# Kernel optimization log

Hardware: AMD Instinct MI355X
Metric: run time of the kernel (lower is better)

Reference implementation:

```python
import jax, jax.numpy as jnp
import numpy as np

N = 50000
E = 800000
H, C = 8, 16          # heads, per-head channels (H*C = 128)
G = 64                # number of graphs
EPS = 1e-5


def setup_inputs() -> dict:
    key = jax.random.key(0)
    ks = jax.random.split(key, 8)
    x = jax.random.normal(ks[0], (N, 128), dtype=jnp.float32)
    edge_index = jax.random.randint(ks[1], (2, E), 0, N, dtype=jnp.int64)
    batch = jnp.sort(jax.random.randint(ks[2], (N,), 0, G, dtype=jnp.int64))
    W = jax.random.normal(ks[3], (3, 128, 128), dtype=jnp.float32) * 0.08
    att_src = jax.random.normal(ks[4], (3, H, C), dtype=jnp.float32) * 0.1
    att_dst = jax.random.normal(ks[5], (3, H, C), dtype=jnp.float32) * 0.1
    bias = jnp.zeros((3, 128), dtype=jnp.float32)
    gamma = jnp.ones((3, 128), dtype=jnp.float32)
    beta = jnp.zeros((3, 128), dtype=jnp.float32)
    ro_w = jax.random.normal(ks[6], (128, 2), dtype=jnp.float32) * 0.08
    ro_b = jnp.zeros((2,), dtype=jnp.float32)
    return {"x": x, "edge_index": edge_index, "batch": batch, "W": W,
            "att_src": att_src, "att_dst": att_dst, "bias": bias,
            "gamma": gamma, "beta": beta, "ro_w": ro_w, "ro_b": ro_b}


def _gat_block(prev, h, src, dst, W, a_s, a_d, b, g, be):
    # GATConv (concat=True, add_self_loops already applied to src/dst)
    xp = (h @ W).reshape(N, H, C)                       # [N,H,C]
    al_s = jnp.sum(xp * a_s, axis=-1)                   # [N,H]
    al_d = jnp.sum(xp * a_d, axis=-1)                   # [N,H]
    logits = jax.nn.leaky_relu(al_s[src] + al_d[dst], negative_slope=0.2)  # [Et,H]
    m = jax.ops.segment_max(logits, dst, num_segments=N)        # softmax over dst groups
    ex = jnp.exp(logits - m[dst])
    denom = jax.ops.segment_sum(ex, dst, num_segments=N)
    alpha = ex / denom[dst]                              # [Et,H]
    msg = xp[src] * alpha[:, :, None]                    # [Et,H,C]
    agg = jax.ops.segment_sum(msg, dst, num_segments=N).reshape(N, H * C) + b
    y = prev + agg
    # BatchNorm1d (training mode: batch stats, biased variance)
    mu = y.mean(axis=0)
    var = y.var(axis=0)
    yn = (y - mu) / jnp.sqrt(var + EPS) * g + be
    return jax.nn.elu(yn)


def reference(x, edge_index, batch, W, att_src, att_dst, bias, gamma, beta, ro_w, ro_b):
    loops = jnp.arange(N, dtype=edge_index.dtype)
    src = jnp.concatenate([edge_index[0], loops])        # PyG add_self_loops=True
    dst = jnp.concatenate([edge_index[1], loops])
    h = x
    prev = jnp.zeros((N, 128), dtype=x.dtype)
    for i in range(3):
        out = _gat_block(prev, h, src, dst, W[i], att_src[i], att_dst[i],
                         bias[i], gamma[i], beta[i])
        prev = h[:, :128]
        h = out
    # global mean pool over graphs
    sums = jax.ops.segment_sum(h, batch, num_segments=G)
    cnt = jax.ops.segment_sum(jnp.ones((N,), dtype=h.dtype), batch, num_segments=G)
    pooled = sums / jnp.maximum(cnt, 1.0)[:, None]
    return pooled @ ro_w + ro_b
```

## Files before the change

kernel.cpp:

```cpp
#include <hip/hip_runtime.h>
#include <hip/hip_bf16.h>
#include <math.h>

#define NN 50000
#define EE 800000
#define MM (EE + NN)
#define GG 64
#define SWG 512
#define NSB ((NN + 255) / 256)
#define PSP 16

__device__ __forceinline__ int geti(const void* p, long idx, int is64) {
    return is64 ? (int)((const long long*)p)[idx] : ((const int*)p)[idx];
}

__device__ __forceinline__ float bf2f(unsigned short u) {
    return __uint_as_float(((unsigned)u) << 16);
}

__device__ __forceinline__ float eluf(float z) {
    return z > 0.f ? z : expm1f(z);
}


__global__ void k_zero(int* p, int n, const int* __restrict__ ei, int* __restrict__ flag) {
    int i = blockIdx.x * blockDim.x + threadIdx.x;
    if (i < n) p[i] = 0;
    if (blockIdx.x == 0 && threadIdx.x == 0 && ei != nullptr) {
        int ok = 1;
        for (int k = 0; k < 128; ++k) {
            int lo = ei[2 * k], hi = ei[2 * k + 1];
            if (hi != 0 || (unsigned)lo >= (unsigned)NN) { ok = 0; break; }
        }
        flag[0] = ok;
    }
}

__global__ void k_count(const void* __restrict__ ei, const int* __restrict__ flag,
                        int* __restrict__ counts) {
    int e = blockIdx.x * blockDim.x + threadIdx.x;
    if (e >= MM) return;
    int is64 = flag[0];
    int d = (e < EE) ? geti(ei, (long)EE + e, is64) : (e - EE);
    if ((unsigned)d < (unsigned)NN) atomicAdd(&counts[d], 1);
}

__global__ __launch_bounds__(256) void k_scan1(const int* __restrict__ counts,
                                               int* __restrict__ rowptr,
                                               int* __restrict__ bsum) {
    __shared__ int buf[256];
    int b = blockIdx.x, tid = threadIdx.x;
    int i = b * 256 + tid;
    int v = (i < NN) ? counts[i] : 0;
    buf[tid] = v;
    __syncthreads();
    for (int off = 1; off < 256; off <<= 1) {
        int t = (tid >= off) ? buf[tid - off] : 0;
        __syncthreads();
        buf[tid] += t;
        __syncthreads();
    }
    if (i < NN) rowptr[i + 1] = buf[tid];
    if (tid == 255) bsum[b] = buf[255];
}

__global__ __launch_bounds__(256) void k_scan2(int* __restrict__ bsum) {
    __shared__ int buf[256];
    int tid = threadIdx.x;
    int v = (tid < NSB) ? bsum[tid] : 0;
    buf[tid] = v;
    __syncthreads();
    for (int off = 1; off < 256; off <<= 1) {
        int t = (tid >= off) ? buf[tid - off] : 0;
        __syncthreads();
        buf[tid] += t;
        __syncthreads();
    }
    if (tid < NSB) bsum[tid] = (tid == 0) ? 0 : buf[tid - 1];
}

__global__ __launch_bounds__(256) void k_scan3(int* __restrict__ rowptr,
                                               const int* __restrict__ bsum) {
    int b = blockIdx.x, tid = threadIdx.x;
    int i = b * 256 + tid;
    if (i < NN) rowptr[i + 1] += bsum[b];
    if (b == 0 && tid == 0) rowptr[0] = 0;
}

__global__ void k_fill(const void* __restrict__ ei, const int* __restrict__ flag,
                       const int* __restrict__ rowptr,
                       int* __restrict__ fill, int* __restrict__ colv) {
    int e = blockIdx.x * blockDim.x + threadIdx.x;
    if (e >= MM) return;
    int is64 = flag[0];
    int s, d;
    if (e < EE) { s = geti(ei, e, is64); d = geti(ei, (long)EE + e, is64); }
    else { s = d = e - EE; }
    if ((unsigned)d >= (unsigned)NN || (unsigned)s >= (unsigned)NN) return;
    int pos = rowptr[d] + atomicAdd(&fill[d], 1);
    if ((unsigned)pos < (unsigned)MM) colv[pos] = s;
}


__global__ __launch_bounds__(256) void k_gemm_att(
    const float* __restrict__ hsrc, const float* __restrict__ Ysrc,
    const float* __restrict__ st, const float* __restrict__ W,
    const float* __restrict__ attS, const float* __restrict__ attD,
    unsigned short* __restrict__ xpb, float* __restrict__ als,
    float* __restrict__ ald, int n)
{
    __shared__ float Wt[32][8][12];
    __shared__ float Ht[128][34];
    int tid = threadIdx.x;
    int hh = tid & 7;
    int r0 = tid >> 3;
    int rbase = (blockIdx.x >> 1) * 128;
    int cbase = (blockIdx.x & 1) * 64;
    bool useY = (Ysrc != nullptr);

    float acc[4][8];
#pragma unroll
    for (int a = 0; a < 4; ++a)
#pragma unroll
        for (int b = 0; b < 8; ++b) acc[a][b] = 0.f;

    for (int k0 = 0; k0 < 128; k0 += 32) {
#pragma unroll
        for (int jj = 0; jj < 2; ++jj) {
            int idx = tid * 2 + jj;
            int kk = idx >> 4;
            int cpos = (idx & 15) * 4;
            int h2 = cpos >> 3, t = cpos & 7;
            *(float4*)&Wt[kk][h2][t] =
                *(const float4*)&W[(k0 + kk) * 128 + cbase + h2 * 8 + t];
        }
#pragma unroll
        for (int j = 0; j < 4; ++j) {
            int f = tid * 16 + j * 4;
            int r = f >> 5, kk = f & 31;
            int gr = rbase + r;
            float4 v = make_float4(0.f, 0.f, 0.f, 0.f);
            if (gr < n) {
                if (useY) {
                    float4 yv = *(const float4*)&Ysrc[gr * 128 + k0 + kk];
                    float4 scv = *(const float4*)&st[k0 + kk];
                    float4 shv = *(const float4*)&st[128 + k0 + kk];
                    v.x = eluf(fmaf(yv.x, scv.x, shv.x));
                    v.y = eluf(fmaf(yv.y, scv.y, shv.y));
                    v.z = eluf(fmaf(yv.z, scv.z, shv.z));
                    v.w = eluf(fmaf(yv.w, scv.w, shv.w));
                } else {
                    v = *(const float4*)&hsrc[gr * 128 + k0 + kk];
                }
            }
            Ht[r][kk] = v.x; Ht[r][kk + 1] = v.y; Ht[r][kk + 2] = v.z; Ht[r][kk + 3] = v.w;
        }
        __syncthreads();
#pragma unroll 2
        for (int kk = 0; kk < 32; kk += 2) {
            float wv0[8], wv1[8];
            *(float4*)&wv0[0] = *(const float4*)&Wt[kk][hh][0];
            *(float4*)&wv0[4] = *(const float4*)&Wt[kk][hh][4];
            *(float4*)&wv1[0] = *(const float4*)&Wt[kk + 1][hh][0];
            *(float4*)&wv1[4] = *(const float4*)&Wt[kk + 1][hh][4];
#pragma unroll
            for (int rr = 0; rr < 4; ++rr) {
                float2 hv = *(const float2*)&Ht[r0 + rr * 32][kk];
#pragma unroll
                for (int j = 0; j < 8; ++j) {
                    acc[rr][j] = fmaf(hv.x, wv0[j], acc[rr][j]);
                    acc[rr][j] = fmaf(hv.y, wv1[j], acc[rr][j]);
                }
            }
        }
        __syncthreads();
    }

    int head = (cbase >> 4) + (hh >> 1);
    int halfsel = hh & 1;
    float asv[8], adv[8];
#pragma unroll
    for (int j = 0; j < 8; ++j) {
        asv[j] = attS[head * 16 + halfsel * 8 + j];
        adv[j] = attD[head * 16 + halfsel * 8 + j];
    }

#pragma unroll
    for (int rr = 0; rr < 4; ++rr) {
        int r = rbase + r0 + rr * 32;
        if (r < n) {
            float ds = 0.f, dd = 0.f;
#pragma unroll
            for (int j = 0; j < 8; ++j) { ds = fmaf(acc[rr][j], asv[j], ds); dd = fmaf(acc[rr][j], adv[j], dd); }
            ds += __shfl_xor(ds, 1);
            dd += __shfl_xor(dd, 1);
            if (halfsel == 0) {
                als[r * 8 + head] = ds;
                ald[r * 8 + head] = dd;
            }
            unsigned short xb[8];
#pragma unroll
            for (int j = 0; j < 8; ++j) {
                __hip_bfloat16 t = __float2bfloat16(acc[rr][j]);
                xb[j] = *reinterpret_cast<unsigned short*>(&t);
            }
            *(uint4*)&xpb[(size_t)r * 128 + cbase + hh * 8] = *(uint4*)&xb[0];
        }
    }
}


__global__ __launch_bounds__(256) void k_agg(
    const unsigned short* __restrict__ xpb, const float* __restrict__ als,
    const float* __restrict__ ald,
    const int* __restrict__ rowptr, const int* __restrict__ colv,
    const float* __restrict__ prevRaw, const float* __restrict__ prevY,
    const float* __restrict__ pst, const float* __restrict__ bias,
    float* __restrict__ y, int n)
{
    int wid = (int)((blockIdx.x * blockDim.x + threadIdx.x) >> 6);
    int lane = threadIdx.x & 63;
    if (wid >= n) return;
    int rs = rowptr[wid], re = rowptr[wid + 1];
    int deg = re - rs;

    int hd = lane & 7;
    int ee = lane >> 3;
    float aldn = ald[wid * 8 + hd];
    int q = ee;
    int c0 = lane * 2;

    float a0 = 0.f, a1 = 0.f, smloc = 0.f;
    int full = deg & ~7;

    int se = 0; float va = 0.f;
    if (full > 0) {
        se = colv[rs + ee];
        va = als[se * 8 + hd];
    }

    for (int b0 = 0; b0 < full; b0 += 8) {
        int se_n = 0; float va_n = 0.f;
        if (b0 + 8 < full) {
            se_n = colv[rs + b0 + 8 + ee];
            va_n = als[se_n * 8 + hd];
        }
        float v = va + aldn;
        v = v > 0.f ? v : 0.2f * v;
        float al = expf(v);
        smloc += al;
#pragma unroll
        for (int j = 0; j < 8; ++j) {
            float a = __shfl(al, j * 8 + q);
            int s = __shfl(se, j * 8);
            ushort2 xv = *(const ushort2*)(xpb + (size_t)s * 128 + c0);
            a0 = fmaf(a, bf2f(xv.x), a0);
            a1 = fmaf(a, bf2f(xv.y), a1);
        }
        se = se_n; va = va_n;
    }

    if (full < deg) {
        int nb = deg - full;
        float al = 0.f;
        int se2 = 0;
        if (ee < nb) {
            se2 = colv[rs + full + ee];
            float v = als[se2 * 8 + hd] + aldn;
            v = v > 0.f ? v : 0.2f * v;
            al = expf(v);
            smloc += al;
        }
        for (int j = 0; j < nb; ++j) {
            float a = __shfl(al, j * 8 + q);
            int s = __shfl(se2, j * 8);
            ushort2 xv = *(const ushort2*)(xpb + (size_t)s * 128 + c0);
            a0 = fmaf(a, bf2f(xv.x), a0);
            a1 = fmaf(a, bf2f(xv.y), a1);
        }
    }

    smloc += __shfl_xor(smloc, 8);
    smloc += __shfl_xor(smloc, 16);
    smloc += __shfl_xor(smloc, 32);
    float inv = 1.f / __shfl(smloc, q);
    a0 *= inv;
    a1 *= inv;

    float p0 = 0.f, p1 = 0.f;
    if (prevY) {
        float2 yv = *(const float2*)(prevY + (size_t)wid * 128 + c0);
        p0 = eluf(fmaf(yv.x, pst[c0], pst[128 + c0]));
        p1 = eluf(fmaf(yv.y, pst[c0 + 1], pst[129 + c0]));
    } else if (prevRaw) {
        p0 = prevRaw[(size_t)wid * 128 + c0];
        p1 = prevRaw[(size_t)wid * 128 + c0 + 1];
    }
    y[wid * 128 + c0] = p0 + a0 + bias[c0];
    y[wid * 128 + c0 + 1] = p1 + a1 + bias[c0 + 1];
}


__global__ __launch_bounds__(256) void k_stats(const float* __restrict__ y,
                                               double* __restrict__ partial, int n) {
    int col = threadIdx.x & 127;
    int rg = threadIdx.x >> 7;
    double s = 0.0, s2 = 0.0;
    for (int r = blockIdx.x * 2 + rg; r < n; r += SWG * 2) {
        float v = y[r * 128 + col];
        s += v; s2 += (double)v * (double)v;
    }
    __shared__ double ls[256], ls2[256];
    ls[threadIdx.x] = s; ls2[threadIdx.x] = s2;
    __syncthreads();
    if (rg == 0) {
        s += ls[threadIdx.x + 128];
        s2 += ls2[threadIdx.x + 128];
        partial[col * SWG + blockIdx.x] = s;
        partial[128 * SWG + col * SWG + blockIdx.x] = s2;
    }
}

__global__ void k_stats_fin(const double* __restrict__ partial,
                            const float* __restrict__ gamma,
                            const float* __restrict__ beta,
                            float* __restrict__ st, int n) {
    int col = threadIdx.x;
    double s = 0.0, s2 = 0.0;
    for (int w = 0; w < SWG; ++w) {
        s += partial[col * SWG + w];
        s2 += partial[128 * SWG + col * SWG + w];
    }
    double mu = s / n;
    double var = s2 / n - mu * mu;
    double rsig = 1.0 / sqrt(var + 1e-5);
    double sc = (double)gamma[col] * rsig;
    st[col] = (float)sc;
    st[128 + col] = (float)((double)beta[col] - mu * sc);
}


__global__ __launch_bounds__(256) void k_pool_part(
    const float* __restrict__ Y, const float* __restrict__ st,
    const void* __restrict__ batch, const int* __restrict__ flag,
    float* __restrict__ ppart, int n)
{
    int g = blockIdx.x / PSP;
    int sp = blockIdx.x % PSP;
    int is64 = flag[0];
    int lo = 0, hi = n;
    while (lo < hi) { int mid = (lo + hi) >> 1; if (geti(batch, mid, is64) < g) lo = mid + 1; else hi = mid; }
    int start = lo;
    hi = n;
    while (lo < hi) { int mid = (lo + hi) >> 1; if (geti(batch, mid, is64) < g + 1) lo = mid + 1; else hi = mid; }
    int end = lo;
    int cnt = end - start;
    int slice = (cnt + PSP - 1) / PSP;
    int s0 = start + sp * slice;
    int s1 = s0 + slice; if (s1 > end) s1 = end;

    int col = threadIdx.x & 127;
    int half = threadIdx.x >> 7;
    float sc = st[col], sh = st[128 + col];
    float s = 0.f;
    for (int r = s0 + half; r < s1; r += 2)
        s += eluf(fmaf(Y[(size_t)r * 128 + col], sc, sh));
    __shared__ float ls[256];
    ls[threadIdx.x] = s;
    __syncthreads();
    if (half == 0) ppart[(g * PSP + sp) * 128 + col] = s + ls[col + 128];
}

__global__ __launch_bounds__(128) void k_pool_fin(
    const float* __restrict__ ppart, const void* __restrict__ batch,
    const int* __restrict__ flag, const float* __restrict__ row,
    const float* __restrict__ rob, float* __restrict__ out, int n)
{
    int g = blockIdx.x;
    int is64 = flag[0];
    int lo = 0, hi = n;
    while (lo < hi) { int mid = (lo + hi) >> 1; if (geti(batch, mid, is64) < g) lo = mid + 1; else hi = mid; }
    int start = lo;
    hi = n;
    while (lo < hi) { int mid = (lo + hi) >> 1; if (geti(batch, mid, is64) < g + 1) lo = mid + 1; else hi = mid; }
    int cnt = lo - start;

    int col = threadIdx.x;
    float s = 0.f;
#pragma unroll
    for (int sp = 0; sp < PSP; ++sp) s += ppart[(g * PSP + sp) * 128 + col];
    __shared__ float ls[128];
    ls[col] = s * (1.f / fmaxf((float)cnt, 1.f));
    __syncthreads();
    if (col < 2) {
        float acc = 0.f;
        for (int c = 0; c < 128; ++c) acc = fmaf(ls[c], row[c * 2 + col], acc);
        out[g * 2 + col] = acc + rob[col];
    }
}


extern "C" void kernel_launch(void* const* d_in, const int* in_sizes, int n_in,
                              void* d_out, int out_size, void* d_ws, size_t ws_size,
                              hipStream_t stream) {
    const float* x     = (const float*)d_in[0];
    const void*  ei    = d_in[1];
    const void*  batch = d_in[2];
    const float* W     = (const float*)d_in[3];
    const float* attS  = (const float*)d_in[4];
    const float* attD  = (const float*)d_in[5];
    const float* bias  = (const float*)d_in[6];
    const float* gamma = (const float*)d_in[7];
    const float* beta  = (const float*)d_in[8];
    const float* row   = (const float*)d_in[9];
    const float* rob   = (const float*)d_in[10];
    float* out = (float*)d_out;

    char* wsb = (char*)d_ws;
    size_t off = 0;
    auto alloc = [&](size_t bytes) {
        void* p = wsb + off;
        off += (bytes + 255) & ~(size_t)255;
        return p;
    };
    int*    flag    = (int*)alloc(256);
    int*    rowptr  = (int*)alloc((size_t)(NN + 1) * 4);
    int*    cnts    = (int*)alloc((size_t)NN * 4 * 2);
    int*    bsum    = (int*)alloc((size_t)256 * 4);
    int*    colv    = (int*)alloc((size_t)MM * 4);
    double* partial = (double*)alloc((size_t)128 * SWG * 2 * 8);
    float*  st1     = (float*)alloc(256 * 4);
    float*  st2     = (float*)alloc(256 * 4);
    float*  st3     = (float*)alloc(256 * 4);
    float*  ppart   = (float*)alloc((size_t)GG * PSP * 128 * 4);
    float*  ALS     = (float*)alloc((size_t)NN * 8 * 4);
    float*  ALD     = (float*)alloc((size_t)NN * 8 * 4);
    unsigned short* XPB = (unsigned short*)alloc((size_t)NN * 128 * 2);
    float* Y1 = (float*)alloc((size_t)NN * 128 * 4);
    float* Y2 = (float*)alloc((size_t)NN * 128 * 4);
    float* Y3 = (float*)alloc((size_t)NN * 128 * 4);
    (void)ws_size; (void)in_sizes; (void)n_in; (void)out_size;

    int* fill = cnts + NN;
    const int GB2 = ((NN + 127) / 128) * 2;
    const int GA = (NN + 3) / 4;

    hipLaunchKernelGGL(k_zero, dim3((2 * NN + 255) / 256), dim3(256), 0, stream,
                       cnts, 2 * NN, (const int*)ei, flag);
    hipLaunchKernelGGL(k_count, dim3((MM + 255) / 256), dim3(256), 0, stream, ei, flag, cnts);
    hipLaunchKernelGGL(k_scan1, dim3(NSB), dim3(256), 0, stream, cnts, rowptr, bsum);
    hipLaunchKernelGGL(k_scan2, dim3(1), dim3(256), 0, stream, bsum);
    hipLaunchKernelGGL(k_scan3, dim3(NSB), dim3(256), 0, stream, rowptr, bsum);
    hipLaunchKernelGGL(k_fill, dim3((MM + 255) / 256), dim3(256), 0, stream, ei, flag, rowptr, fill, colv);

    hipLaunchKernelGGL(k_gemm_att, dim3(GB2), dim3(256), 0, stream,
                       x, (const float*)nullptr, (const float*)nullptr,
                       W, attS, attD, XPB, ALS, ALD, NN);
    hipLaunchKernelGGL(k_agg, dim3(GA), dim3(256), 0, stream,
                       XPB, ALS, ALD, rowptr, colv,
                       (const float*)nullptr, (const float*)nullptr, (const float*)nullptr,
                       bias, Y1, NN);
    hipLaunchKernelGGL(k_stats, dim3(SWG), dim3(256), 0, stream, Y1, partial, NN);
    hipLaunchKernelGGL(k_stats_fin, dim3(1), dim3(128), 0, stream, partial, gamma, beta, st1, NN);

    hipLaunchKernelGGL(k_gemm_att, dim3(GB2), dim3(256), 0, stream,
                       (const float*)nullptr, Y1, st1,
                       W + 16384, attS + 128, attD + 128, XPB, ALS, ALD, NN);
    hipLaunchKernelGGL(k_agg, dim3(GA), dim3(256), 0, stream,
                       XPB, ALS, ALD, rowptr, colv,
                       x, (const float*)nullptr, (const float*)nullptr,
                       bias + 128, Y2, NN);
    hipLaunchKernelGGL(k_stats, dim3(SWG), dim3(256), 0, stream, Y2, partial, NN);
    hipLaunchKernelGGL(k_stats_fin, dim3(1), dim3(128), 0, stream, partial, gamma + 128, beta + 128, st2, NN);

    hipLaunchKernelGGL(k_gemm_att, dim3(GB2), dim3(256), 0, stream,
                       (const float*)nullptr, Y2, st2,
                       W + 32768, attS + 256, attD + 256, XPB, ALS, ALD, NN);
    hipLaunchKernelGGL(k_agg, dim3(GA), dim3(256), 0, stream,
                       XPB, ALS, ALD, rowptr, colv,
                       (const float*)nullptr, Y1, st1,
                       bias + 256, Y3, NN);
    hipLaunchKernelGGL(k_stats, dim3(SWG), dim3(256), 0, stream, Y3, partial, NN);
    hipLaunchKernelGGL(k_stats_fin, dim3(1), dim3(128), 0, stream, partial, gamma + 256, beta + 256, st3, NN);

    hipLaunchKernelGGL(k_pool_part, dim3(GG * PSP), dim3(256), 0, stream,
                       Y3, st3, batch, flag, ppart, NN);
    hipLaunchKernelGGL(k_pool_fin, dim3(GG), dim3(128), 0, stream,
                       ppart, batch, flag, row, rob, out, NN);
}
```

Before: 539.3 us.

## Use bf16 MFMA for node projection GEMM with prepacked weights

Replaces the FP32 FMA-based projection GEMM with bf16 MFMA 16x16x32 instructions. A new kernel converts all three weight matrices once per call into an MFMA operand layout, and each block now computes a full 64-row by 128-column tile from a bf16 copy of the input rows staged in shared memory. The attention dot products are computed from the MFMA accumulators using cross-lane shuffles. This cuts GEMM compute time but rounds the inputs and weights to bf16, adding error, and the scalar 2-byte output stores are less coalesced than the previous 16-byte stores.

```diff
diff --git a/kernel.cpp b/kernel.cpp
--- a/kernel.cpp
+++ b/kernel.cpp
@@ -10,12 +10,20 @@
 #define NSB ((NN + 255) / 256)
 #define PSP 16
 
+typedef __attribute__((ext_vector_type(8))) short short8v;
+typedef __attribute__((ext_vector_type(4))) float float4v;
+
 __device__ __forceinline__ int geti(const void* p, long idx, int is64) {
     return is64 ? (int)((const long long*)p)[idx] : ((const int*)p)[idx];
 }
 
 __device__ __forceinline__ float bf2f(unsigned short u) {
     return __uint_as_float(((unsigned)u) << 16);
+}
+
+__device__ __forceinline__ unsigned short f2bf(float f) {
+    __hip_bfloat16 t = __float2bfloat16(f);
+    return *reinterpret_cast<unsigned short*>(&t);
 }
 
 __device__ __forceinline__ float eluf(float z) {
@@ -102,109 +110,95 @@
 }
 
 
+__global__ __launch_bounds__(256) void k_packW(const float* __restrict__ W,
+                                               unsigned short* __restrict__ Wpk) {
+    int idx = blockIdx.x * 256 + threadIdx.x;
+    if (idx >= 3 * 2048) return;
+    int l = idx & 63, ct = (idx >> 6) & 7, ks = (idx >> 9) & 3, L = idx >> 11;
+    const float* Wb = W + L * 16384;
+    int c = ct * 16 + (l & 15);
+    int kbase = ks * 32 + (l >> 4) * 8;
+    unsigned short v[8];
+#pragma unroll
+    for (int j = 0; j < 8; ++j) v[j] = f2bf(Wb[(kbase + j) * 128 + c]);
+    *(uint4*)(Wpk + (size_t)idx * 8) = *(uint4*)v;
+}
+
+
 __global__ __launch_bounds__(256) void k_gemm_att(
     const float* __restrict__ hsrc, const float* __restrict__ Ysrc,
-    const float* __restrict__ st, const float* __restrict__ W,
+    const float* __restrict__ st, const unsigned short* __restrict__ Wpk,
     const float* __restrict__ attS, const float* __restrict__ attD,
     unsigned short* __restrict__ xpb, float* __restrict__ als,
     float* __restrict__ ald, int n)
 {
-    __shared__ float Wt[32][8][12];
-    __shared__ float Ht[128][34];
+    __shared__ unsigned short Hb[64][136];
     int tid = threadIdx.x;
-    int hh = tid & 7;
-    int r0 = tid >> 3;
-    int rbase = (blockIdx.x >> 1) * 128;
-    int cbase = (blockIdx.x & 1) * 64;
+    int wv = tid >> 6, lane = tid & 63;
+    int rbase = blockIdx.x * 64;
     bool useY = (Ysrc != nullptr);
 
-    float acc[4][8];
-#pragma unroll
-    for (int a = 0; a < 4; ++a)
-#pragma unroll
-        for (int b = 0; b < 8; ++b) acc[a][b] = 0.f;
-
-    for (int k0 = 0; k0 < 128; k0 += 32) {
-#pragma unroll
-        for (int jj = 0; jj < 2; ++jj) {
-            int idx = tid * 2 + jj;
-            int kk = idx >> 4;
-            int cpos = (idx & 15) * 4;
-            int h2 = cpos >> 3, t = cpos & 7;
-            *(float4*)&Wt[kk][h2][t] =
-                *(const float4*)&W[(k0 + kk) * 128 + cbase + h2 * 8 + t];
-        }
-#pragma unroll
-        for (int j = 0; j < 4; ++j) {
-            int f = tid * 16 + j * 4;
-            int r = f >> 5, kk = f & 31;
-            int gr = rbase + r;
-            float4 v = make_float4(0.f, 0.f, 0.f, 0.f);
-            if (gr < n) {
-                if (useY) {
-                    float4 yv = *(const float4*)&Ysrc[gr * 128 + k0 + kk];
-                    float4 scv = *(const float4*)&st[k0 + kk];
-                    float4 shv = *(const float4*)&st[128 + k0 + kk];
-                    v.x = eluf(fmaf(yv.x, scv.x, shv.x));
-                    v.y = eluf(fmaf(yv.y, scv.y, shv.y));
-                    v.z = eluf(fmaf(yv.z, scv.z, shv.z));
-                    v.w = eluf(fmaf(yv.w, scv.w, shv.w));
-                } else {
-                    v = *(const float4*)&hsrc[gr * 128 + k0 + kk];
-                }
+#pragma unroll
+    for (int i = 0; i < 8; ++i) {
+        int idx = i * 256 + tid;
+        int row = idx >> 5;
+        int kq = (idx & 31) * 4;
+        int gr = rbase + row;
+        float4 v = make_float4(0.f, 0.f, 0.f, 0.f);
+        if (gr < n) {
+            if (useY) {
+                float4 yv = *(const float4*)&Ysrc[(size_t)gr * 128 + kq];
+                float4 scv = *(const float4*)&st[kq];
+                float4 shv = *(const float4*)&st[128 + kq];
+                v.x = eluf(fmaf(yv.x, scv.x, shv.x));
+                v.y = eluf(fmaf(yv.y, scv.y, shv.y));
+                v.z = eluf(fmaf(yv.z, scv.z, shv.z));
+                v.w = eluf(fmaf(yv.w, scv.w, shv.w));
+            } else {
+                v = *(const float4*)&hsrc[(size_t)gr * 128 + kq];
             }
-            Ht[r][kk] = v.x; Ht[r][kk + 1] = v.y; Ht[r][kk + 2] = v.z; Ht[r][kk + 3] = v.w;
-        }
-        __syncthreads();
-#pragma unroll 2
-        for (int kk = 0; kk < 32; kk += 2) {
-            float wv0[8], wv1[8];
-            *(float4*)&wv0[0] = *(const float4*)&Wt[kk][hh][0];
-            *(float4*)&wv0[4] = *(const float4*)&Wt[kk][hh][4];
-            *(float4*)&wv1[0] = *(const float4*)&Wt[kk + 1][hh][0];
-            *(float4*)&wv1[4] = *(const float4*)&Wt[kk + 1][hh][4];
-#pragma unroll
-            for (int rr = 0; rr < 4; ++rr) {
-                float2 hv = *(const float2*)&Ht[r0 + rr * 32][kk];
-#pragma unroll
-                for (int j = 0; j < 8; ++j) {
-                    acc[rr][j] = fmaf(hv.x, wv0[j], acc[rr][j]);
-                    acc[rr][j] = fmaf(hv.y, wv1[j], acc[rr][j]);
-                }
+        }
+        ushort4 b;
+        b.x = f2bf(v.x); b.y = f2bf(v.y); b.z = f2bf(v.z); b.w = f2bf(v.w);
+        *(ushort4*)&Hb[row][kq] = b;
+    }
+    __syncthreads();
+
+    int g = lane >> 4, c15 = lane & 15;
+
+    float4v acc[8];
+#pragma unroll
+    for (int ct = 0; ct < 8; ++ct) acc[ct] = (float4v)(0.f);
+
+#pragma unroll
+    for (int ks = 0; ks < 4; ++ks) {
+        short8v a = *(const short8v*)&Hb[wv * 16 + c15][ks * 32 + g * 8];
+#pragma unroll
+        for (int ct = 0; ct < 8; ++ct) {
+            short8v b = *(const short8v*)(Wpk + (((size_t)(ks * 8 + ct) * 64 + lane) * 8));
+            acc[ct] = __builtin_amdgcn_mfma_f32_16x16x32_bf16(a, b, acc[ct], 0, 0, 0);
+        }
+    }
+
+#pragma unroll
+    for (int ct = 0; ct < 8; ++ct) {
+        float as_ = attS[ct * 16 + c15];
+        float ad_ = attD[ct * 16 + c15];
+#pragma unroll
+        for (int r = 0; r < 4; ++r) {
+            int row = rbase + wv * 16 + g * 4 + r;
+            float val = acc[ct][r];
+            if (row < n) xpb[(size_t)row * 128 + ct * 16 + c15] = f2bf(val);
+            float ds = val * as_;
+            float dd = val * ad_;
+            ds += __shfl_xor(ds, 1); ds += __shfl_xor(ds, 2);
+            ds += __shfl_xor(ds, 4); ds += __shfl_xor(ds, 8);
+            dd += __shfl_xor(dd, 1); dd += __shfl_xor(dd, 2);
+            dd += __shfl_xor(dd, 4); dd += __shfl_xor(dd, 8);
+            if (c15 == 0 && row < n) {
+                als[row * 8 + ct] = ds;
+                ald[row * 8 + ct] = dd;
             }
-        }
-        __syncthreads();
-    }
-
-    int head = (cbase >> 4) + (hh >> 1);
-    int halfsel = hh & 1;
-    float asv[8], adv[8];
-#pragma unroll
-    for (int j = 0; j < 8; ++j) {
-        asv[j] = attS[head * 16 + halfsel * 8 + j];
-        adv[j] = attD[head * 16 + halfsel * 8 + j];
-    }
-
-#pragma unroll
-    for (int rr = 0; rr < 4; ++rr) {
-        int r = rbase + r0 + rr * 32;
-        if (r < n) {
-            float ds = 0.f, dd = 0.f;
-#pragma unroll
-            for (int j = 0; j < 8; ++j) { ds = fmaf(acc[rr][j], asv[j], ds); dd = fmaf(acc[rr][j], adv[j], dd); }
-            ds += __shfl_xor(ds, 1);
-            dd += __shfl_xor(dd, 1);
-            if (halfsel == 0) {
-                als[r * 8 + head] = ds;
-                ald[r * 8 + head] = dd;
-            }
-            unsigned short xb[8];
-#pragma unroll
-            for (int j = 0; j < 8; ++j) {
-                __hip_bfloat16 t = __float2bfloat16(acc[rr][j]);
-                xb[j] = *reinterpret_cast<unsigned short*>(&t);
-            }
-            *(uint4*)&xpb[(size_t)r * 128 + cbase + hh * 8] = *(uint4*)&xb[0];
         }
     }
 }
@@ -436,26 +430,28 @@
     float*  ALS     = (float*)alloc((size_t)NN * 8 * 4);
     float*  ALD     = (float*)alloc((size_t)NN * 8 * 4);
     unsigned short* XPB = (unsigned short*)alloc((size_t)NN * 128 * 2);
+    unsigned short* WPK = (unsigned short*)alloc((size_t)3 * 2048 * 8 * 2);
     float* Y1 = (float*)alloc((size_t)NN * 128 * 4);
     float* Y2 = (float*)alloc((size_t)NN * 128 * 4);
     float* Y3 = (float*)alloc((size_t)NN * 128 * 4);
     (void)ws_size; (void)in_sizes; (void)n_in; (void)out_size;
 
     int* fill = cnts + NN;
-    const int GB2 = ((NN + 127) / 128) * 2;
+    const int GBM = (NN + 63) / 64;
     const int GA = (NN + 3) / 4;
 
     hipLaunchKernelGGL(k_zero, dim3((2 * NN + 255) / 256), dim3(256), 0, stream,
                        cnts, 2 * NN, (const int*)ei, flag);
+    hipLaunchKernelGGL(k_packW, dim3(24), dim3(256), 0, stream, W, WPK);
     hipLaunchKernelGGL(k_count, dim3((MM + 255) / 256), dim3(256), 0, stream, ei, flag, cnts);
     hipLaunchKernelGGL(k_scan1, dim3(NSB), dim3(256), 0, stream, cnts, rowptr, bsum);
     hipLaunchKernelGGL(k_scan2, dim3(1), dim3(256), 0, stream, bsum);
     hipLaunchKernelGGL(k_scan3, dim3(NSB), dim3(256), 0, stream, rowptr, bsum);
     hipLaunchKernelGGL(k_fill, dim3((MM + 255) / 256), dim3(256), 0, stream, ei, flag, rowptr, fill, colv);
 
-    hipLaunchKernelGGL(k_gemm_att, dim3(GB2), dim3(256), 0, stream,
+    hipLaunchKernelGGL(k_gemm_att, dim3(GBM), dim3(256), 0, stream,
                        x, (const float*)nullptr, (const float*)nullptr,
-                       W, attS, attD, XPB, ALS, ALD, NN);
+                       WPK, attS, attD, XPB, ALS, ALD, NN);
     hipLaunchKernelGGL(k_agg, dim3(GA), dim3(256), 0, stream,
                        XPB, ALS, ALD, rowptr, colv,
                        (const float*)nullptr, (const float*)nullptr, (const float*)nullptr,
@@ -463,9 +459,9 @@
     hipLaunchKernelGGL(k_stats, dim3(SWG), dim3(256), 0, stream, Y1, partial, NN);
     hipLaunchKernelGGL(k_stats_fin, dim3(1), dim3(128), 0, stream, partial, gamma, beta, st1, NN);
 
-    hipLaunchKernelGGL(k_gemm_att, dim3(GB2), dim3(256), 0, stream,
+    hipLaunchKernelGGL(k_gemm_att, dim3(GBM), dim3(256), 0, stream,
                        (const float*)nullptr, Y1, st1,
-                       W + 16384, attS + 128, attD + 128, XPB, ALS, ALD, NN);
+                       WPK + (size_t)2048 * 8, attS + 128, attD + 128, XPB, ALS, ALD, NN);
     hipLaunchKernelGGL(k_agg, dim3(GA), dim3(256), 0, stream,
                        XPB, ALS, ALD, rowptr, colv,
                        x, (const float*)nullptr, (const float*)nullptr,
@@ -473,9 +469,9 @@
     hipLaunchKernelGGL(k_stats, dim3(SWG), dim3(256), 0, stream, Y2, partial, NN);
     hipLaunchKernelGGL(k_stats_fin, dim3(1), dim3(128), 0, stream, partial, gamma + 128, beta + 128, st2, NN);
 
-    hipLaunchKernelGGL(k_gemm_att, dim3(GB2), dim3(256), 0, stream,
+    hipLaunchKernelGGL(k_gemm_att, dim3(GBM), dim3(256), 0, stream,
                        (const float*)nullptr, Y2, st2,
-                       W + 32768, attS + 256, attD + 256, XPB, ALS, ALD, NN);
+                       WPK + (size_t)2 * 2048 * 8, attS + 256, attD + 256, XPB, ALS, ALD, NN);
     hipLaunchKernelGGL(k_agg, dim3(GA), dim3(256), 0, stream,
                        XPB, ALS, ALD, rowptr, colv,
                        (const float*)nullptr, Y1, st1,
```

Result: faster. 490.5 us (-9.1%).
